# Performance work log

Measured on AMD Instinct MI355X. Metric: run time of the kernel, lower is better.

## Reference

```python
import jax, jax.numpy as jnp
import numpy as np

T, B, IN_DIM, H = 512, 64, 1024, 1024

def setup_inputs() -> dict:
    key = jax.random.key(0)
    kx, kwx, kwh = jax.random.split(key, 3)
    x = jax.random.normal(kx, (T, B, IN_DIM), dtype=jnp.float32)
    # lecun_normal: std = 1/sqrt(fan_in)
    W_x = jax.random.normal(kwx, (IN_DIM, 4 * H), dtype=jnp.float32) / np.sqrt(IN_DIM)
    W_h = jax.random.normal(kwh, (H, 4 * H), dtype=jnp.float32) / np.sqrt(H)
    b = jnp.zeros((4 * H,), dtype=jnp.float32)
    return {"x": x, "W_x": W_x, "W_h": W_h, "b": b}

def reference(x, W_x, W_h, b):
    Tn, Bn, _ = x.shape
    Hn = W_h.shape[0]
    h0 = jnp.zeros((Bn, Hn), dtype=x.dtype)
    c0 = jnp.zeros((Bn, Hn), dtype=x.dtype)

    def step(carry, xt):
        h, c = carry
        gates = xt @ W_x + h @ W_h + b  # [B, 4H]
        i, f, g, o = jnp.split(gates, 4, axis=-1)
        i = jax.nn.sigmoid(i)
        f = jax.nn.sigmoid(f)
        o = jax.nn.sigmoid(o)
        g = jnp.tanh(g)
        c_new = f * c + i * g
        h_new = o * jnp.tanh(c_new)
        return (h_new, c_new), h_new

    (hT, cT), hs = jax.lax.scan(step, (h0, c0), x)
    return hs, (hT, cT)
```

## Files before the change

### kernel.cpp

```cpp
#include <hip/hip_runtime.h>

typedef unsigned short u16;
typedef unsigned int u32;
typedef unsigned long long u64;
typedef float f32x4 __attribute__((ext_vector_type(4)));
typedef __bf16 bf16x8 __attribute__((ext_vector_type(8)));
typedef u16 u16x8 __attribute__((ext_vector_type(8)));

#define T_STEPS 512
#define BATCH 64
#define HDIM 1024
#define GDIM 4096
#define HS_ELEMS (33554432u)
#define XP_STEP 262144

__device__ __forceinline__ u16 f2bf(float f) {
  union { float f; u32 u; } v; v.f = f;
  u32 r = v.u + 0x7fffu + ((v.u >> 16) & 1u);
  return (u16)(r >> 16);
}
__device__ __forceinline__ float bf2f(u16 b) {
  union { u32 u; float f; } v; v.u = ((u32)b) << 16;
  return v.f;
}
__device__ __forceinline__ float sigm(float x) { return 1.f / (1.f + __expf(-x)); }
__device__ __forceinline__ float tanh_fast(float x) { return 1.f - 2.f / (__expf(2.f * x) + 1.f); }

__global__ void transpose_w(const float* __restrict__ Wx, const float* __restrict__ Wh,
                            u16* __restrict__ WxT, u16* __restrict__ WhT) {
  __shared__ float tile[32][33];
  const float* src = blockIdx.z ? Wh : Wx;
  u16* dst = blockIdx.z ? WhT : WxT;
  const int n0 = blockIdx.x * 32, k0 = blockIdx.y * 32;
  const int tx = threadIdx.x, ty = threadIdx.y;
#pragma unroll
  for (int i = 0; i < 4; ++i)
    tile[ty + i * 8][tx] = src[(size_t)(k0 + ty + i * 8) * GDIM + n0 + tx];
  __syncthreads();
#pragma unroll
  for (int i = 0; i < 4; ++i)
    dst[(size_t)(n0 + ty + i * 8) * HDIM + k0 + tx] = f2bf(tile[tx][ty + i * 8]);
}

__global__ __launch_bounds__(256, 2) void gemm_xp(
    const float* __restrict__ X, const u16* __restrict__ WxT,
    const float* __restrict__ bias, u16* __restrict__ Xp) {
  __shared__ u16 As[128 * 40];
  __shared__ u16 Bs[128 * 40];
  const int tid = threadIdx.x;
  const int lane = tid & 63, w = tid >> 6;
  const int rl = lane & 15, gq = lane >> 4, g8 = gq * 8;
  const int swz = (blockIdx.x & 7) * 1024 + (blockIdx.x >> 3);
  const int m0 = (swz >> 5) * 128, n0 = (swz & 31) * 128;
  const int srow = tid >> 1, sseg = (tid & 1) * 16;
  const int rbase = (w >> 1) * 64, cbase = (w & 1) * 64;

  f32x4 acc[4][4] = {};
  for (int k0 = 0; k0 < 1024; k0 += 32) {
    const float4* ap = (const float4*)&X[(size_t)(m0 + srow) * 1024 + k0 + sseg];
    float4 v0 = ap[0], v1 = ap[1], v2 = ap[2], v3 = ap[3];
    u16x8 pa, pb;
    pa[0] = f2bf(v0.x); pa[1] = f2bf(v0.y); pa[2] = f2bf(v0.z); pa[3] = f2bf(v0.w);
    pa[4] = f2bf(v1.x); pa[5] = f2bf(v1.y); pa[6] = f2bf(v1.z); pa[7] = f2bf(v1.w);
    pb[0] = f2bf(v2.x); pb[1] = f2bf(v2.y); pb[2] = f2bf(v2.z); pb[3] = f2bf(v2.w);
    pb[4] = f2bf(v3.x); pb[5] = f2bf(v3.y); pb[6] = f2bf(v3.z); pb[7] = f2bf(v3.w);
    const u16x8* bp = (const u16x8*)&WxT[(size_t)(n0 + srow) * 1024 + k0 + sseg];
    u16x8 qa = bp[0], qb = bp[1];
    *(u16x8*)&As[srow * 40 + sseg] = pa;
    *(u16x8*)&As[srow * 40 + sseg + 8] = pb;
    *(u16x8*)&Bs[srow * 40 + sseg] = qa;
    *(u16x8*)&Bs[srow * 40 + sseg + 8] = qb;
    __syncthreads();
    bf16x8 av[4], bv[4];
#pragma unroll
    for (int i = 0; i < 4; ++i)
      av[i] = *(const bf16x8*)&As[(rbase + i * 16 + rl) * 40 + g8];
#pragma unroll
    for (int j = 0; j < 4; ++j)
      bv[j] = *(const bf16x8*)&Bs[(cbase + j * 16 + rl) * 40 + g8];
#pragma unroll
    for (int i = 0; i < 4; ++i)
#pragma unroll
      for (int j = 0; j < 4; ++j)
        acc[i][j] = __builtin_amdgcn_mfma_f32_16x16x32_bf16(av[i], bv[j], acc[i][j], 0, 0, 0);
    __syncthreads();
  }
#pragma unroll
  for (int j = 0; j < 4; ++j) {
    const int n = n0 + cbase + j * 16 + rl;
    const float bj = bias[n];
    const int gate = n >> 10, col = n & 1023;
    const int cri = col >> 5, hcoli = col & 31;
#pragma unroll
    for (int i = 0; i < 4; ++i)
#pragma unroll
      for (int r = 0; r < 4; ++r) {
        const int m = m0 + rbase + i * 16 + gq * 4 + r;
        const int tt = m >> 6, b = m & 63;
        Xp[(size_t)tt * XP_STEP + (size_t)((b >> 4) * 32 + cri) * 2048 +
           gate * 512 + (b & 15) * 32 + hcoli] = f2bf(acc[i][j][r] + bj);
      }
  }
}

__global__ void zero_tags(u32* __restrict__ ht) {
  const u32 i = blockIdx.x * 256 + threadIdx.x;
  if (i < 131200u) ht[i] = 0;
}

__global__ __launch_bounds__(512, 1) void lstm_rec(
    const u16* __restrict__ Xp, const u16* __restrict__ WhT,
    u32* __restrict__ h_tag, u32* __restrict__ flags, float* __restrict__ out) {
  __shared__ u16 h_lds[16 * 1024];
  __shared__ float gate_lds[4][2][16][20];
  const int tid = threadIdx.x;
  const int lane = tid & 63, w = tid >> 6;
  const int rl = lane & 15, gq = lane >> 4;
  const int cr = blockIdx.x & 31, bg = blockIdx.x >> 5;
  const int g = w >> 1, c2 = w & 1;

  bf16x8 wf[32];
  {
    const size_t gcol = (size_t)(g * 1024 + cr * 32 + c2 * 16 + rl) * HDIM + gq * 8;
#pragma unroll
    for (int kk = 0; kk < 32; ++kk)
      wf[kk] = *(const bf16x8*)&WhT[gcol + kk * 32];
  }

  const int b_el = tid >> 5, hcol = tid & 31;
  const int srow = tid >> 5, s32 = tid & 31;
  const int swz_w = ((srow & 7) << 4) ^ ((srow & 1) << 6);
  const int swz_r = ((rl & 7) << 4) ^ ((rl & 1) << 6);
  float creg = 0.f, hreg = 0.f;

  const u16* xp_p = Xp + (size_t)blockIdx.x * 2048 + tid;
  float xg0 = bf2f(xp_p[0]), xg1 = bf2f(xp_p[512]),
        xg2 = bf2f(xp_p[1024]), xg3 = bf2f(xp_p[1536]);

  const u32* flagrow = flags + bg * 32 + (lane & 31);

  for (int t = 0; t < T_STEPS; ++t) {
    u16 nx0 = 0, nx1 = 0, nx2 = 0, nx3 = 0;
    if (t + 1 < T_STEPS) {
      const u16* p = xp_p + XP_STEP;
      nx0 = p[0]; nx1 = p[512]; nx2 = p[1024]; nx3 = p[1536];
    }

    f32x4 acc0 = {0.f, 0.f, 0.f, 0.f}, acc1 = {0.f, 0.f, 0.f, 0.f};
    if (t > 0) {
      for (;;) {
        u32 f = __hip_atomic_load(flagrow, __ATOMIC_RELAXED, __HIP_MEMORY_SCOPE_AGENT);
        if (__all((int)(f >= (u32)t))) break;
      }
      const u64* hrow =
          (const u64*)(h_tag + (size_t)(t & 1) * 65536 + (size_t)(bg * 16 + srow) * 1024);
      char* ldsrow = (char*)h_lds + srow * 2048;
      u64 v[16];
#pragma unroll
      for (int u = 0; u < 16; ++u)
        v[u] = __hip_atomic_load(&hrow[s32 + 32 * u], __ATOMIC_RELAXED,
                                 __HIP_MEMORY_SCOPE_AGENT);
      u32 pend = 0u;
#pragma unroll
      for (int u = 0; u < 16; ++u) {
        const u32 t0 = (u32)(v[u] >> 16) & 0xffffu, t1 = (u32)(v[u] >> 48);
        const u32 pack = ((u32)v[u] & 0xffffu) | (((u32)(v[u] >> 32) & 0xffffu) << 16);
        *(u32*)(ldsrow + (((s32 + 32 * u) * 4) ^ swz_w)) = pack;
        if (t0 < (u32)t || t1 < (u32)t) pend |= (1u << u);
      }
      while (__builtin_expect(pend != 0u, 0)) {
        const int uu = __ffs(pend) - 1;
        u64 vv = __hip_atomic_load(&hrow[s32 + 32 * uu], __ATOMIC_RELAXED,
                                   __HIP_MEMORY_SCOPE_AGENT);
        const u32 t0 = (u32)(vv >> 16) & 0xffffu, t1 = (u32)(vv >> 48);
        if (t0 >= (u32)t && t1 >= (u32)t) {
          const u32 pack = ((u32)vv & 0xffffu) | (((u32)(vv >> 32) & 0xffffu) << 16);
          *(u32*)(ldsrow + (((s32 + 32 * uu) * 4) ^ swz_w)) = pack;
          pend &= pend - 1u;
        }
      }
      __syncthreads();
      const char* hrd = (const char*)h_lds + rl * 2048;
#pragma unroll
      for (int kk = 0; kk < 32; kk += 2) {
        bf16x8 a0 = *(const bf16x8*)(hrd + ((kk * 64 + gq * 16) ^ swz_r));
        bf16x8 a1 = *(const bf16x8*)(hrd + (((kk + 1) * 64 + gq * 16) ^ swz_r));
        acc0 = __builtin_amdgcn_mfma_f32_16x16x32_bf16(a0, wf[kk], acc0, 0, 0, 0);
        acc1 = __builtin_amdgcn_mfma_f32_16x16x32_bf16(a1, wf[kk + 1], acc1, 0, 0, 0);
      }
      acc0 += acc1;
    } else {
      __syncthreads();
    }
#pragma unroll
    for (int r = 0; r < 4; ++r)
      gate_lds[g][c2][gq * 4 + r][rl] = acc0[r];
    __syncthreads();
    {
      const int cq = hcol >> 4, cl = hcol & 15;
      const float gi = gate_lds[0][cq][b_el][cl] + xg0;
      const float gf = gate_lds[1][cq][b_el][cl] + xg1;
      const float gg = gate_lds[2][cq][b_el][cl] + xg2;
      const float go = gate_lds[3][cq][b_el][cl] + xg3;
      const float iv = sigm(gi);
      const float fv = sigm(gf);
      const float gv = tanh_fast(gg);
      const float ov = sigm(go);
      creg = fv * creg + iv * gv;
      hreg = ov * tanh_fast(creg);
      const u32 wv = (u32)f2bf(hreg) | ((u32)(t + 1) << 16);
      __hip_atomic_store(
          &h_tag[(size_t)((t + 1) & 1) * 65536 + (size_t)(bg * 16 + b_el) * 1024 + cr * 32 + hcol],
          wv, __ATOMIC_RELAXED, __HIP_MEMORY_SCOPE_AGENT);
    }
    if (tid == 0)
      __hip_atomic_store(&flags[bg * 32 + cr], (u32)(t + 1), __ATOMIC_RELAXED,
                         __HIP_MEMORY_SCOPE_AGENT);
    out[((size_t)t * BATCH + bg * 16 + b_el) * HDIM + cr * 32 + hcol] = hreg;
    xg0 = bf2f(nx0); xg1 = bf2f(nx1); xg2 = bf2f(nx2); xg3 = bf2f(nx3);
    xp_p += XP_STEP;
  }
  out[(size_t)HS_ELEMS + (size_t)(bg * 16 + b_el) * HDIM + cr * 32 + hcol] = hreg;
  out[(size_t)HS_ELEMS + 65536u + (size_t)(bg * 16 + b_el) * HDIM + cr * 32 + hcol] = creg;
}

extern "C" void kernel_launch(void* const* d_in, const int* in_sizes, int n_in,
                              void* d_out, int out_size, void* d_ws, size_t ws_size,
                              hipStream_t stream) {
  const float* x = (const float*)d_in[0];
  const float* Wx = (const float*)d_in[1];
  const float* Wh = (const float*)d_in[2];
  const float* bias = (const float*)d_in[3];
  float* out = (float*)d_out;
  char* ws = (char*)d_ws;

  u16* WxT = (u16*)(ws + 0);
  u32* h_tag = (u32*)(ws + 0);
  u32* flags = (u32*)(ws + 524288);
  u16* WhT = (u16*)(ws + 8388608);
  u16* Xp = (u16*)(ws + 16777216);

  transpose_w<<<dim3(128, 32, 2), dim3(32, 8), 0, stream>>>(Wx, Wh, WxT, WhT);
  gemm_xp<<<dim3(8192), dim3(256), 0, stream>>>(x, WxT, bias, Xp);
  zero_tags<<<dim3(514), dim3(256), 0, stream>>>(h_tag);
  lstm_rec<<<dim3(128), dim3(512), 0, stream>>>(Xp, WhT, h_tag, flags, out);
}
```

Before: 2.588 ms.

## Pre-convert x to bf16, use direct-to-LDS loads in GEMM, widen h loads

Adds a separate pass that converts x to bf16 into the output buffer, used as scratch, so the input-projection GEMM can stream bf16 tiles straight into LDS with global_load_lds and no register staging or padding. The recurrent kernel now reads the tagged h values with 16-byte cache-bypassing loads (sc0 sc1) instead of 8-byte atomics, which halves the number of load instructions on the critical per-step path. The trade-offs are an extra full pass over x, unpadded LDS rows that may cause bank conflicts, and inline asm loads that rely on the cache-bypass bits to see fresh data.

```diff
diff --git a/kernel.cpp b/kernel.cpp
--- a/kernel.cpp
+++ b/kernel.cpp
@@ -6,6 +6,7 @@
 typedef float f32x4 __attribute__((ext_vector_type(4)));
 typedef __bf16 bf16x8 __attribute__((ext_vector_type(8)));
 typedef u16 u16x8 __attribute__((ext_vector_type(8)));
+typedef u32 u32x4 __attribute__((ext_vector_type(4)));
 
 #define T_STEPS 512
 #define BATCH 64
@@ -25,6 +26,17 @@
 }
 __device__ __forceinline__ float sigm(float x) { return 1.f / (1.f + __expf(-x)); }
 __device__ __forceinline__ float tanh_fast(float x) { return 1.f - 2.f / (__expf(2.f * x) + 1.f); }
+
+__device__ __forceinline__ void gload16(const void* g, void* l) {
+  __builtin_amdgcn_global_load_lds(
+      (const __attribute__((address_space(1))) u32*)g,
+      (__attribute__((address_space(3))) u32*)l, 16, 0, 0);
+}
+__device__ __forceinline__ u32x4 cload16(const void* g) {
+  u32x4 r;
+  asm volatile("global_load_dwordx4 %0, %1, off sc0 sc1" : "=&v"(r) : "v"(g) : "memory");
+  return r;
+}
 
 __global__ void transpose_w(const float* __restrict__ Wx, const float* __restrict__ Wh,
                             u16* __restrict__ WxT, u16* __restrict__ WhT) {
@@ -42,42 +54,43 @@
     dst[(size_t)(n0 + ty + i * 8) * HDIM + k0 + tx] = f2bf(tile[tx][ty + i * 8]);
 }
 
-__global__ __launch_bounds__(256, 2) void gemm_xp(
-    const float* __restrict__ X, const u16* __restrict__ WxT,
+__global__ void convert_x(const float* __restrict__ X, u16* __restrict__ Xbf) {
+  const size_t i = ((size_t)blockIdx.x * 256 + threadIdx.x) * 8;
+  const float4 a = *(const float4*)&X[i];
+  const float4 b = *(const float4*)&X[i + 4];
+  u16x8 o;
+  o[0] = f2bf(a.x); o[1] = f2bf(a.y); o[2] = f2bf(a.z); o[3] = f2bf(a.w);
+  o[4] = f2bf(b.x); o[5] = f2bf(b.y); o[6] = f2bf(b.z); o[7] = f2bf(b.w);
+  *(u16x8*)&Xbf[i] = o;
+}
+
+__global__ __launch_bounds__(256) void gemm_xp(
+    const u16* __restrict__ Xbf, const u16* __restrict__ WxT,
     const float* __restrict__ bias, u16* __restrict__ Xp) {
-  __shared__ u16 As[128 * 40];
-  __shared__ u16 Bs[128 * 40];
+  __shared__ u16 As[128 * 32];
+  __shared__ u16 Bs[128 * 32];
   const int tid = threadIdx.x;
   const int lane = tid & 63, w = tid >> 6;
   const int rl = lane & 15, gq = lane >> 4, g8 = gq * 8;
   const int swz = (blockIdx.x & 7) * 1024 + (blockIdx.x >> 3);
   const int m0 = (swz >> 5) * 128, n0 = (swz & 31) * 128;
-  const int srow = tid >> 1, sseg = (tid & 1) * 16;
   const int rbase = (w >> 1) * 64, cbase = (w & 1) * 64;
+  const int r0 = tid >> 2, c0 = (tid & 3) * 8;
 
   f32x4 acc[4][4] = {};
   for (int k0 = 0; k0 < 1024; k0 += 32) {
-    const float4* ap = (const float4*)&X[(size_t)(m0 + srow) * 1024 + k0 + sseg];
-    float4 v0 = ap[0], v1 = ap[1], v2 = ap[2], v3 = ap[3];
-    u16x8 pa, pb;
-    pa[0] = f2bf(v0.x); pa[1] = f2bf(v0.y); pa[2] = f2bf(v0.z); pa[3] = f2bf(v0.w);
-    pa[4] = f2bf(v1.x); pa[5] = f2bf(v1.y); pa[6] = f2bf(v1.z); pa[7] = f2bf(v1.w);
-    pb[0] = f2bf(v2.x); pb[1] = f2bf(v2.y); pb[2] = f2bf(v2.z); pb[3] = f2bf(v2.w);
-    pb[4] = f2bf(v3.x); pb[5] = f2bf(v3.y); pb[6] = f2bf(v3.z); pb[7] = f2bf(v3.w);
-    const u16x8* bp = (const u16x8*)&WxT[(size_t)(n0 + srow) * 1024 + k0 + sseg];
-    u16x8 qa = bp[0], qb = bp[1];
-    *(u16x8*)&As[srow * 40 + sseg] = pa;
-    *(u16x8*)&As[srow * 40 + sseg + 8] = pb;
-    *(u16x8*)&Bs[srow * 40 + sseg] = qa;
-    *(u16x8*)&Bs[srow * 40 + sseg + 8] = qb;
+    gload16(&Xbf[(size_t)(m0 + r0) * 1024 + k0 + c0], &As[w * 512]);
+    gload16(&Xbf[(size_t)(m0 + r0 + 64) * 1024 + k0 + c0], &As[2048 + w * 512]);
+    gload16(&WxT[(size_t)(n0 + r0) * 1024 + k0 + c0], &Bs[w * 512]);
+    gload16(&WxT[(size_t)(n0 + r0 + 64) * 1024 + k0 + c0], &Bs[2048 + w * 512]);
     __syncthreads();
     bf16x8 av[4], bv[4];
 #pragma unroll
     for (int i = 0; i < 4; ++i)
-      av[i] = *(const bf16x8*)&As[(rbase + i * 16 + rl) * 40 + g8];
+      av[i] = *(const bf16x8*)&As[(rbase + i * 16 + rl) * 32 + g8];
 #pragma unroll
     for (int j = 0; j < 4; ++j)
-      bv[j] = *(const bf16x8*)&Bs[(cbase + j * 16 + rl) * 40 + g8];
+      bv[j] = *(const bf16x8*)&Bs[(cbase + j * 16 + rl) * 32 + g8];
 #pragma unroll
     for (int i = 0; i < 4; ++i)
 #pragma unroll
@@ -152,30 +165,39 @@
         u32 f = __hip_atomic_load(flagrow, __ATOMIC_RELAXED, __HIP_MEMORY_SCOPE_AGENT);
         if (__all((int)(f >= (u32)t))) break;
       }
-      const u64* hrow =
-          (const u64*)(h_tag + (size_t)(t & 1) * 65536 + (size_t)(bg * 16 + srow) * 1024);
+      const u32* hrow32 =
+          h_tag + (size_t)(t & 1) * 65536 + (size_t)(bg * 16 + srow) * 1024;
       char* ldsrow = (char*)h_lds + srow * 2048;
-      u64 v[16];
-#pragma unroll
-      for (int u = 0; u < 16; ++u)
-        v[u] = __hip_atomic_load(&hrow[s32 + 32 * u], __ATOMIC_RELAXED,
-                                 __HIP_MEMORY_SCOPE_AGENT);
+      u32x4 v[8];
+#pragma unroll
+      for (int u = 0; u < 8; ++u)
+        v[u] = cload16((const char*)hrow32 + 512 * u + 16 * s32);
+      asm volatile("s_waitcnt vmcnt(0)" ::: "memory");
+      __builtin_amdgcn_sched_barrier(0);
       u32 pend = 0u;
 #pragma unroll
-      for (int u = 0; u < 16; ++u) {
-        const u32 t0 = (u32)(v[u] >> 16) & 0xffffu, t1 = (u32)(v[u] >> 48);
-        const u32 pack = ((u32)v[u] & 0xffffu) | (((u32)(v[u] >> 32) & 0xffffu) << 16);
-        *(u32*)(ldsrow + (((s32 + 32 * u) * 4) ^ swz_w)) = pack;
-        if (t0 < (u32)t || t1 < (u32)t) pend |= (1u << u);
+      for (int u = 0; u < 8; ++u) {
+        const u32 w0 = v[u][0], w1 = v[u][1], w2 = v[u][2], w3 = v[u][3];
+        const u64 packs = (u64)((w0 & 0xffffu) | (w1 << 16)) |
+                          ((u64)((w2 & 0xffffu) | (w3 << 16)) << 32);
+        *(u64*)(ldsrow + ((256 * u + 8 * s32) ^ swz_w)) = packs;
+        if ((w0 >> 16) < (u32)t || (w1 >> 16) < (u32)t ||
+            (w2 >> 16) < (u32)t || (w3 >> 16) < (u32)t)
+          pend |= (1u << u);
       }
       while (__builtin_expect(pend != 0u, 0)) {
         const int uu = __ffs(pend) - 1;
-        u64 vv = __hip_atomic_load(&hrow[s32 + 32 * uu], __ATOMIC_RELAXED,
-                                   __HIP_MEMORY_SCOPE_AGENT);
-        const u32 t0 = (u32)(vv >> 16) & 0xffffu, t1 = (u32)(vv >> 48);
-        if (t0 >= (u32)t && t1 >= (u32)t) {
-          const u32 pack = ((u32)vv & 0xffffu) | (((u32)(vv >> 32) & 0xffffu) << 16);
-          *(u32*)(ldsrow + (((s32 + 32 * uu) * 4) ^ swz_w)) = pack;
+        const u64* h64 = (const u64*)hrow32;
+        const int j0 = 64 * uu + 2 * s32;
+        u64 a = __hip_atomic_load(&h64[j0], __ATOMIC_RELAXED, __HIP_MEMORY_SCOPE_AGENT);
+        u64 b = __hip_atomic_load(&h64[j0 + 1], __ATOMIC_RELAXED, __HIP_MEMORY_SCOPE_AGENT);
+        const u32 t0 = (u32)(a >> 16) & 0xffffu, t1 = (u32)(a >> 48);
+        const u32 t2 = (u32)(b >> 16) & 0xffffu, t3 = (u32)(b >> 48);
+        if (t0 >= (u32)t && t1 >= (u32)t && t2 >= (u32)t && t3 >= (u32)t) {
+          const u64 packs =
+              (u64)(((u32)a & 0xffffu) | (((u32)(a >> 32) & 0xffffu) << 16)) |
+              ((u64)(((u32)b & 0xffffu) | (((u32)(b >> 32) & 0xffffu) << 16)) << 32);
+          *(u64*)(ldsrow + ((256 * uu + 8 * s32) ^ swz_w)) = packs;
           pend &= pend - 1u;
         }
       }
@@ -239,9 +261,11 @@
   u32* flags = (u32*)(ws + 524288);
   u16* WhT = (u16*)(ws + 8388608);
   u16* Xp = (u16*)(ws + 16777216);
+  u16* Xbf = (u16*)d_out;
 
   transpose_w<<<dim3(128, 32, 2), dim3(32, 8), 0, stream>>>(Wx, Wh, WxT, WhT);
-  gemm_xp<<<dim3(8192), dim3(256), 0, stream>>>(x, WxT, bias, Xp);
+  convert_x<<<dim3(16384), dim3(256), 0, stream>>>(x, Xbf);
+  gemm_xp<<<dim3(8192), dim3(256), 0, stream>>>(Xbf, WxT, bias, Xp);
   zero_tags<<<dim3(514), dim3(256), 0, stream>>>(h_tag);
   lstm_rec<<<dim3(128), dim3(512), 0, stream>>>(Xp, WhT, h_tag, flags, out);
 }
```

Measured after the change: 2.267 ms. -12.4%, faster.
